# Kernel optimization log

Hardware: AMD Instinct MI355X
Metric: run time of the kernel (lower is better)

Reference implementation:

```python
import jax, jax.numpy as jnp
import numpy as np

NUM_K_HEADS = 16
NUM_V_HEADS = 32
DK = 128
DV = 128
KCONV = 4
EPS = 1e-6
KEY_DIM = NUM_K_HEADS * DK      # 2048
VALUE_DIM = NUM_V_HEADS * DV    # 4096
HIDDEN = 2048
T_TOKENS = 4096


def setup_inputs() -> dict:
    key = jax.random.key(0)
    ks = jax.random.split(key, 10)
    s = 0.02
    return {
        "hidden_states": jax.random.normal(ks[0], (T_TOKENS, HIDDEN), jnp.float32),
        "W_qkv": jax.random.normal(ks[1], (2 * KEY_DIM + VALUE_DIM, HIDDEN), jnp.float32) * s,
        "W_z": jax.random.normal(ks[2], (VALUE_DIM, HIDDEN), jnp.float32) * s,
        "W_b": jax.random.normal(ks[3], (NUM_V_HEADS, HIDDEN), jnp.float32) * s,
        "W_a": jax.random.normal(ks[4], (NUM_V_HEADS, HIDDEN), jnp.float32) * s,
        "conv_weight": jax.random.normal(ks[5], (2 * KEY_DIM + VALUE_DIM, KCONV), jnp.float32) * 0.2,
        "dt_bias": jnp.ones((NUM_V_HEADS,), jnp.float32),
        "A_log": jax.random.normal(ks[6], (NUM_V_HEADS,), jnp.float32) * 0.5,
        "norm_weight": jnp.ones((DV,), jnp.float32),
        "W_out": jax.random.normal(ks[7], (HIDDEN, VALUE_DIM), jnp.float32) * s,
    }


def _l2norm(x):
    return x * jax.lax.rsqrt(jnp.sum(x * x, axis=-1, keepdims=True) + 1e-6)


def _gdn_forward(hidden_states, W_qkv, W_z, W_b, W_a, conv_weight,
                 dt_bias, A_log, norm_weight, W_out):
    T = hidden_states.shape[0]
    # input projections
    mixed_qkv = hidden_states @ W_qkv.T                         # [T, 2K+V]
    z = (hidden_states @ W_z.T).reshape(T, NUM_V_HEADS, DV)     # gate
    b = hidden_states @ W_b.T                                   # [T, Hv]
    a = hidden_states @ W_a.T                                   # [T, Hv]

    # depthwise causal conv1d (kernel 4) + silu, no bias
    xp = jnp.pad(mixed_qkv, ((KCONV - 1, 0), (0, 0)))
    conv = sum(xp[i:i + T] * conv_weight[:, i] for i in range(KCONV))
    x = jax.nn.silu(conv)

    q = x[:, :KEY_DIM].reshape(T, NUM_K_HEADS, DK)
    k = x[:, KEY_DIM:2 * KEY_DIM].reshape(T, NUM_K_HEADS, DK)
    v = x[:, 2 * KEY_DIM:].reshape(T, NUM_V_HEADS, DV)

    rep = NUM_V_HEADS // NUM_K_HEADS  # grouped value attention: repeat q/k heads
    q = jnp.repeat(_l2norm(q), rep, axis=1)  # [T, Hv, DK]
    k = jnp.repeat(_l2norm(k), rep, axis=1)

    beta = jax.nn.sigmoid(b)                                   # [T, Hv]
    g = -jnp.exp(A_log) * jax.nn.softplus(a + dt_bias)         # [T, Hv] log-decay
    scale = DK ** -0.5

    def step(S, inp):
        qt, kt, vt, bt, gt = inp
        S = S * jnp.exp(gt)[:, None, None]                     # gated decay
        kv = jnp.einsum('hk,hkv->hv', kt, S)                   # memory readout
        delta = (vt - kv) * bt[:, None]                        # delta rule update
        S = S + jnp.einsum('hk,hv->hkv', kt, delta)
        ot = jnp.einsum('hk,hkv->hv', qt, S) * scale
        return S, ot

    S0 = jnp.zeros((NUM_V_HEADS, DK, DV), mixed_qkv.dtype)
    _, o = jax.lax.scan(step, S0, (q, k, v, beta, g))          # o: [T, Hv, DV]

    # gated RMSNorm (norm before gate)
    var = jnp.mean(o * o, axis=-1, keepdims=True)
    on = o * jax.lax.rsqrt(var + EPS) * norm_weight
    y = on * jax.nn.silu(z)

    return y.reshape(T, VALUE_DIM) @ W_out.T                   # [T, HIDDEN]


def reference(hidden_states, W_qkv, W_z, W_b, W_a, conv_weight,
              dt_bias, A_log, norm_weight, W_out):
    return _gdn_forward(hidden_states, W_qkv, W_z, W_b, W_a, conv_weight,
                        dt_bias, A_log, norm_weight, W_out)
```

## Files before the change

kernel.cpp:

```cpp
#include <hip/hip_runtime.h>
#include <cstdint>
#include <cstddef>

typedef __bf16 bf16_t;
typedef __bf16 bf16x8 __attribute__((ext_vector_type(8)));
typedef __bf16 bf16x4 __attribute__((ext_vector_type(4)));
typedef float floatx4 __attribute__((ext_vector_type(4)));

__device__ __forceinline__ void async16(const bf16_t* g, bf16_t* l) {
  __builtin_amdgcn_global_load_lds(
      (const __attribute__((address_space(1))) unsigned int*)g,
      (__attribute__((address_space(3))) unsigned int*)l, 16, 0, 0);
}

__device__ __forceinline__ void barrier_lds() {
  asm volatile("s_waitcnt lgkmcnt(0)\n\ts_barrier" ::: "memory");
}

__device__ __forceinline__ float siluf(float x) { return x / (1.f + __expf(-x)); }

#define MFMA16(a, b, c) __builtin_amdgcn_mfma_f32_16x16x32_bf16(a, b, c, 0, 0, 0)
#define WAITV(n) asm volatile("s_waitcnt vmcnt(" #n ")" ::: "memory")
#define SBAR() asm volatile("s_barrier" ::: "memory")

__global__ __launch_bounds__(256) void k_cvt(const float* __restrict__ in,
                                             bf16_t* __restrict__ out, int n4) {
  int i = blockIdx.x * 256 + threadIdx.x;
  if (i >= n4) return;
  const float4 f = ((const float4*)in)[i];
  bf16x4 r;
  r[0] = (bf16_t)f.x; r[1] = (bf16_t)f.y; r[2] = (bf16_t)f.z; r[3] = (bf16_t)f.w;
  ((bf16x4*)out)[i] = r;
}

__global__ __launch_bounds__(256) void k_build_wba(const float* __restrict__ wb,
                                                   const float* __restrict__ wa,
                                                   bf16_t* __restrict__ out) {
  int i = blockIdx.x * 256 + threadIdx.x;
  int e = i * 4;
  int row = e >> 11;
  int col = e & 2047;
  float4 f = make_float4(0.f, 0.f, 0.f, 0.f);
  if (row < 32)      f = *(const float4*)&wb[row * 2048 + col];
  else if (row < 64) f = *(const float4*)&wa[(row - 32) * 2048 + col];
  bf16x4 r;
  r[0] = (bf16_t)f.x; r[1] = (bf16_t)f.y; r[2] = (bf16_t)f.z; r[3] = (bf16_t)f.w;
  *(bf16x4*)&out[e] = r;
}

template<bool OUT_BF16>
__global__ __launch_bounds__(256) void gemm_bt(const bf16_t* __restrict__ A,
                                               const bf16_t* __restrict__ B,
                                               void* __restrict__ Cout,
                                               int M, int N, int K) {
  __shared__ __align__(16) bf16_t As[4096];
  __shared__ __align__(16) bf16_t Bs[4096];
  const int tid  = threadIdx.x;
  const int lane = tid & 63;
  const int wave = tid >> 6;
  const int quad = lane >> 4;
  const int l16  = lane & 15;
  const int wr   = (wave >> 1) * 64;
  const int wc   = (wave & 1) * 64;
  const int m0   = blockIdx.y * 128;
  const int n0   = blockIdx.x * 128;
  const int ra   = tid >> 2;
  const int ca   = (tid & 3) * 8;

  const bf16_t* gA = A + (size_t)(m0 + ra) * K + ca;
  const bf16_t* gB = B + (size_t)(n0 + ra) * K + ca;
  bf16_t* lA = &As[tid * 8];
  bf16_t* lB = &Bs[tid * 8];

  floatx4 acc[4][4] = {};

  for (int k0 = 0; k0 < K; k0 += 32) {
    __syncthreads();
    async16(gA + k0, lA);
    async16(gA + k0 + (size_t)64 * K, lA + 2048);
    async16(gB + k0, lB);
    async16(gB + k0 + (size_t)64 * K, lB + 2048);
    __syncthreads();
    bf16x8 af[4], bfr[4];
#pragma unroll
    for (int i = 0; i < 4; ++i) {
      af[i]  = *(const bf16x8*)&As[(wr + i * 16 + l16) * 32 + quad * 8];
      bfr[i] = *(const bf16x8*)&Bs[(wc + i * 16 + l16) * 32 + quad * 8];
    }
#pragma unroll
    for (int mi = 0; mi < 4; ++mi)
#pragma unroll
      for (int ni = 0; ni < 4; ++ni)
        acc[mi][ni] = MFMA16(af[mi], bfr[ni], acc[mi][ni]);
  }

#pragma unroll
  for (int mi = 0; mi < 4; ++mi) {
#pragma unroll
    for (int ni = 0; ni < 4; ++ni) {
      const int row = m0 + wr + mi * 16 + quad * 4;
      const int col = n0 + wc + ni * 16 + l16;
#pragma unroll
      for (int r = 0; r < 4; ++r) {
        if (OUT_BF16)
          ((bf16_t*)Cout)[(size_t)(row + r) * N + col] = (bf16_t)acc[mi][ni][r];
        else
          ((float*)Cout)[(size_t)(row + r) * N + col] = acc[mi][ni][r];
      }
    }
  }
}

__global__ __launch_bounds__(512, 1) void gemm8p(const bf16_t* __restrict__ A,
                                                 const bf16_t* __restrict__ B,
                                                 bf16_t* __restrict__ C0,
                                                 bf16_t* __restrict__ C1,
                                                 int M, int N, int K, int NSPLIT) {
  extern __shared__ __align__(16) bf16_t sm[];
  const int tid  = threadIdx.x;
  const int lane = tid & 63;
  const int wave = tid >> 6;
  const int quad = lane >> 4;
  const int l16  = lane & 15;
  const int wm   = wave >> 2;
  const int wn   = wave & 3;

  const int gx  = (int)gridDim.x;
  const int nwg = gx * (int)gridDim.y;
  const int id  = (int)blockIdx.y * gx + (int)blockIdx.x;
  const int cpx = nwg >> 3;
  const int sw  = (id & 7) * cpx + (id >> 3);
  const int m0  = (sw / gx) * 256;
  const int n0  = (sw % gx) * 256;

  const int rowg   = tid >> 3;
  const int colsrc = (tid & 7) ^ (rowg & 7);
  const bf16_t* gAs = A + (size_t)(m0 + rowg) * K + colsrc * 8;
  const bf16_t* gBs = B + (size_t)(n0 + rowg) * K + colsrc * 8;
  bf16_t* lds0 = sm + tid * 8;

#define STG_A8(u, kt, ht) {                                     \
    bf16_t* la = lds0 + (u) * 32768 + (ht) * 8192;              \
    const bf16_t* ga = gAs + (size_t)(ht) * 128 * K + (kt) * 64;\
    async16(ga, la); async16(ga + (size_t)64 * K, la + 4096); }
#define STG_B8(u, kt, ht) {                                     \
    bf16_t* lb = lds0 + (u) * 32768 + 16384 + (ht) * 8192;      \
    const bf16_t* gb = gBs + (size_t)(ht) * 128 * K + (kt) * 64;\
    async16(gb, lb); async16(gb + (size_t)64 * K, lb + 4096); }

  const int x7  = l16 & 7;
  const int cA0 = ((quad + 0) ^ x7) * 8;
  const int cA1 = ((quad + 4) ^ x7) * 8;
  const int eA0 = (wm * 128 + l16) * 64;
  const int eB0 = 16384 + (wn * 64 + l16) * 64;

  floatx4 acc[8][4] = {};
  const int KT = K >> 6;

  STG_A8(0, 0, 0); STG_A8(0, 0, 1);
  STG_B8(0, 0, 0); STG_B8(0, 0, 1);
  STG_B8(1, 1, 0); STG_B8(1, 1, 1);
  WAITV(4);
  SBAR();

  bf16x8 af[4][2], bn0[2][2], bn1[2][2];
  for (int X = 0; X < KT; ++X) {
    const int c = X & 1;
    const bf16_t* sb = sm + c * 32768;

#pragma unroll
    for (int i = 0; i < 4; ++i) {
      af[i][0] = *(const bf16x8*)&sb[eA0 + i * 1024 + cA0];
      af[i][1] = *(const bf16x8*)&sb[eA0 + i * 1024 + cA1];
    }
#pragma unroll
    for (int j = 0; j < 2; ++j) {
      bn0[j][0] = *(const bf16x8*)&sb[eB0 + j * 1024 + cA0];
      bn0[j][1] = *(const bf16x8*)&sb[eB0 + j * 1024 + cA1];
    }
    if (X + 1 < KT) STG_A8(c ^ 1, X + 1, 0);
    SBAR();
    __builtin_amdgcn_s_setprio(1);
#pragma unroll
    for (int i = 0; i < 4; ++i)
#pragma unroll
      for (int j = 0; j < 2; ++j) {
        acc[i][j] = MFMA16(af[i][0], bn0[j][0], acc[i][j]);
        acc[i][j] = MFMA16(af[i][1], bn0[j][1], acc[i][j]);
      }
    __builtin_amdgcn_s_setprio(0);
    SBAR();

#pragma unroll
    for (int j = 0; j < 2; ++j) {
      bn1[j][0] = *(const bf16x8*)&sb[eB0 + (2 + j) * 1024 + cA0];
      bn1[j][1] = *(const bf16x8*)&sb[eB0 + (2 + j) * 1024 + cA1];
    }
    if (X + 1 < KT) STG_A8(c ^ 1, X + 1, 1);
    SBAR();
    __builtin_amdgcn_s_setprio(1);
#pragma unroll
    for (int i = 0; i < 4; ++i)
#pragma unroll
      for (int j = 0; j < 2; ++j) {
        acc[i][2 + j] = MFMA16(af[i][0], bn1[j][0], acc[i][2 + j]);
        acc[i][2 + j] = MFMA16(af[i][1], bn1[j][1], acc[i][2 + j]);
      }
    __builtin_amdgcn_s_setprio(0);
    SBAR();

#pragma unroll
    for (int i = 0; i < 4; ++i) {
      af[i][0] = *(const bf16x8*)&sb[eA0 + (4 + i) * 1024 + cA0];
      af[i][1] = *(const bf16x8*)&sb[eA0 + (4 + i) * 1024 + cA1];
    }
    if (X + 2 < KT) STG_B8(c, X + 2, 0);
    SBAR();
    __builtin_amdgcn_s_setprio(1);
#pragma unroll
    for (int i = 0; i < 4; ++i)
#pragma unroll
      for (int j = 0; j < 2; ++j) {
        acc[4 + i][j] = MFMA16(af[i][0], bn0[j][0], acc[4 + i][j]);
        acc[4 + i][j] = MFMA16(af[i][1], bn0[j][1], acc[4 + i][j]);
      }
    __builtin_amdgcn_s_setprio(0);
    SBAR();

    if (X + 2 < KT) { STG_B8(c, X + 2, 1); WAITV(4); }
    else            { WAITV(0); }
    SBAR();
    __builtin_amdgcn_s_setprio(1);
#pragma unroll
    for (int i = 0; i < 4; ++i)
#pragma unroll
      for (int j = 0; j < 2; ++j) {
        acc[4 + i][2 + j] = MFMA16(af[i][0], bn1[j][0], acc[4 + i][2 + j]);
        acc[4 + i][2 + j] = MFMA16(af[i][1], bn1[j][1], acc[4 + i][2 + j]);
      }
    __builtin_amdgcn_s_setprio(0);
    SBAR();
  }
#undef STG_A8
#undef STG_B8

  const bool lo = (n0 < NSPLIT);
  bf16_t* Cb = lo ? C0 : C1;
  const int pitch = lo ? NSPLIT : (N - NSPLIT);
  const int ncol0 = lo ? n0 : (n0 - NSPLIT);
#pragma unroll
  for (int mi = 0; mi < 8; ++mi) {
#pragma unroll
    for (int ni = 0; ni < 4; ++ni) {
      const int row = m0 + wm * 128 + mi * 16 + quad * 4;
      const int col = ncol0 + wn * 64 + ni * 16 + l16;
#pragma unroll
      for (int r = 0; r < 4; ++r)
        Cb[(size_t)(row + r) * pitch + col] = (bf16_t)acc[mi][ni][r];
    }
  }
}

template<int MH, bool OUT_BF16>
__global__ __launch_bounds__(512, 1) void gemm_big(const bf16_t* __restrict__ A,
                                                   const bf16_t* __restrict__ B,
                                                   void* __restrict__ Cout,
                                                   int M, int N, int K) {
  extern __shared__ __align__(16) bf16_t sm[];
  constexpr int BM    = MH * 128;
  constexpr int MFRAG = MH * 4;
  constexpr int HF    = MFRAG / 2;
  constexpr int BUFE  = MH * 4096 + 8192;
  const int tid  = threadIdx.x;
  const int lane = tid & 63;
  const int wave = tid >> 6;
  const int quad = lane >> 4;
  const int l16  = lane & 15;
  const int wm   = wave >> 2;
  const int wn   = wave & 3;

  const int gx  = (int)gridDim.x;
  const int nwg = gx * (int)gridDim.y;
  const int id  = (int)blockIdx.y * gx + (int)blockIdx.x;
  const int cpx = nwg >> 3;
  const int sw  = (id & 7) * cpx + (id >> 3);
  const int m0  = (sw / gx) * BM;
  const int n0  = (sw % gx) * 256;

  const int lr    = lane >> 2;
  const int lslot = (lane & 3) ^ ((lane >> 3) & 3);
  const bf16_t* gA = A + (size_t)(m0 + wave * (MH * 16) + lr) * K + lslot * 8;
  const bf16_t* gB = B + (size_t)(n0 + wave * 32 + lr) * K + lslot * 8;
  const int ldsA0 = wave * (MH * 512) + lane * 8;
  const int ldsB0 = MH * 4096 + wave * 1024 + lane * 8;

#define STG_A(u, kt) {                                          \
    bf16_t* la = sm + (u) * BUFE + ldsA0;                       \
    const bf16_t* ga = gA + (size_t)(kt) * 32;                  \
    async16(ga, la);                                            \
    if constexpr (MH == 2) async16(ga + (size_t)16 * K, la + 512); }
#define STG_B(u, kt) {                                          \
    bf16_t* lb = sm + (u) * BUFE + ldsB0;                       \
    const bf16_t* gb = gB + (size_t)(kt) * 32;                  \
    async16(gb, lb);                                            \
    async16(gb + (size_t)16 * K, lb + 512); }

  int offA[MFRAG], offB[4];
#pragma unroll
  for (int i = 0; i < MFRAG; ++i) {
    int ra = wm * (MFRAG * 16) + i * 16 + l16;
    offA[i] = (ra * 32 + quad * 8) ^ (((ra >> 1) & 3) << 3);
  }
#pragma unroll
  for (int i = 0; i < 4; ++i) {
    int rb = wn * 64 + i * 16 + l16;
    offB[i] = MH * 4096 + ((rb * 32 + quad * 8) ^ (((rb >> 1) & 3) << 3));
  }

  floatx4 acc[MFRAG][4] = {};
  const int KT = K >> 5;

  STG_A(0, 0); STG_B(0, 0);
  STG_A(1, 1); STG_B(1, 1);
  STG_A(2, 2); STG_B(2, 2);
  if constexpr (MH == 2) WAITV(8); else WAITV(6);
  SBAR();

  for (int U = 0; U < KT; ++U) {
    const int bu = U & 3;
    const bf16_t* sb = sm + bu * BUFE;
    const int un = U + 3;
    const int tu = un & 3;
    bf16x8 af[HF], bfr[4];

#pragma unroll
    for (int i = 0; i < HF; ++i) af[i] = *(const bf16x8*)&sb[offA[i]];
#pragma unroll
    for (int i = 0; i < 4; ++i) bfr[i] = *(const bf16x8*)&sb[offB[i]];
    if (un < KT) STG_A(tu, un);
    SBAR();
    __builtin_amdgcn_s_setprio(1);
#pragma unroll
    for (int mi = 0; mi < HF; ++mi)
#pragma unroll
      for (int ni = 0; ni < 4; ++ni)
        acc[mi][ni] = MFMA16(af[mi], bfr[ni], acc[mi][ni]);
    __builtin_amdgcn_s_setprio(0);
    SBAR();

#pragma unroll
    for (int i = 0; i < HF; ++i) af[i] = *(const bf16x8*)&sb[offA[HF + i]];
    if (un < KT) STG_B(tu, un);
    if (un < KT)         { if constexpr (MH == 2) WAITV(8); else WAITV(6); }
    else if (U + 2 < KT) { if constexpr (MH == 2) WAITV(4); else WAITV(3); }
    else                 WAITV(0);
    SBAR();
    __builtin_amdgcn_s_setprio(1);
#pragma unroll
    for (int mi = 0; mi < HF; ++mi)
#pragma unroll
      for (int ni = 0; ni < 4; ++ni)
        acc[HF + mi][ni] = MFMA16(af[mi], bfr[ni], acc[HF + mi][ni]);
    __builtin_amdgcn_s_setprio(0);
    SBAR();
  }
#undef STG_A
#undef STG_B

#pragma unroll
  for (int mi = 0; mi < MFRAG; ++mi) {
#pragma unroll
    for (int ni = 0; ni < 4; ++ni) {
      const int row = m0 + wm * (MFRAG * 16) + mi * 16 + quad * 4;
      const int col = n0 + wn * 64 + ni * 16 + l16;
#pragma unroll
      for (int r = 0; r < 4; ++r) {
        if (OUT_BF16)
          ((bf16_t*)Cout)[(size_t)(row + r) * N + col] = (bf16_t)acc[mi][ni][r];
        else
          ((float*)Cout)[(size_t)(row + r) * N + col] = acc[mi][ni][r];
      }
    }
  }
}

__global__ __launch_bounds__(256) void k_betag(const float* __restrict__ cba,
                                               const float* __restrict__ A_log,
                                               const float* __restrict__ dtb,
                                               float* __restrict__ beta_t,
                                               float* __restrict__ g_t) {
  int i = blockIdx.x * 256 + threadIdx.x;
  int t = i >> 5, h = i & 31;
  float b = cba[t * 128 + h];
  float a = cba[t * 128 + 32 + h];
  beta_t[h * 4096 + t] = 1.f / (1.f + __expf(-b));
  float x = a + dtb[h];
  float sp = (x > 20.f) ? x : log1pf(__expf(x));
  g_t[h * 4096 + t] = -__expf(A_log[h]) * sp;
}

__global__ __launch_bounds__(64) void k_conv(const bf16_t* __restrict__ mixed,
                                             const float* __restrict__ cw,
                                             bf16_t* __restrict__ qo,
                                             bf16_t* __restrict__ ko,
                                             bf16_t* __restrict__ vo) {
  const int grp = blockIdx.x;
  const int t0 = blockIdx.y * 8;
  const int l = threadIdx.x;
  const int c0 = grp * 128 + l;
  const int c1 = c0 + 64;
  const float4 w0 = *(const float4*)&cw[c0 * 4];
  const float4 w1 = *(const float4*)&cw[c1 * 4];
  float h0[3], h1[3];
#pragma unroll
  for (int j = 0; j < 3; ++j) {
    int tt = t0 - 3 + j;
    h0[j] = (tt >= 0) ? (float)mixed[(size_t)tt * 8192 + c0] : 0.f;
    h1[j] = (tt >= 0) ? (float)mixed[(size_t)tt * 8192 + c1] : 0.f;
  }
#pragma unroll
  for (int i = 0; i < 8; ++i) {
    const int t = t0 + i;
    float x0 = (float)mixed[(size_t)t * 8192 + c0];
    float x1 = (float)mixed[(size_t)t * 8192 + c1];
    float a0 = w0.x * h0[0] + w0.y * h0[1] + w0.z * h0[2] + w0.w * x0;
    float a1 = w1.x * h1[0] + w1.y * h1[1] + w1.z * h1[2] + w1.w * x1;
    h0[0] = h0[1]; h0[1] = h0[2]; h0[2] = x0;
    h1[0] = h1[1]; h1[1] = h1[2]; h1[2] = x1;
    float v0 = siluf(a0), v1 = siluf(a1);
    if (grp < 32) {
      float s = v0 * v0 + v1 * v1;
#pragma unroll
      for (int m = 1; m < 64; m <<= 1) s += __shfl_xor(s, m);
      float r = rsqrtf(s + 1e-6f);
      if (grp < 16) {
        bf16_t* q = qo + ((size_t)t * 16 + grp) * 128;
        q[l]      = (bf16_t)(v0 * r * 0.08838834764831845f);
        q[l + 64] = (bf16_t)(v1 * r * 0.08838834764831845f);
      } else {
        bf16_t* k = ko + ((size_t)t * 16 + grp - 16) * 128;
        k[l]      = (bf16_t)(v0 * r);
        k[l + 64] = (bf16_t)(v1 * r);
      }
    } else {
      bf16_t* v = vo + ((size_t)t * 32 + grp - 32) * 128;
      v[l]      = (bf16_t)v0;
      v[l + 64] = (bf16_t)v1;
    }
  }
}

__global__ __launch_bounds__(256, 2) void k_prep(
    const bf16_t* __restrict__ qg, const bf16_t* __restrict__ kg,
    const bf16_t* __restrict__ vg,
    const float* __restrict__ bb_t, const float* __restrict__ gb_t,
    bf16_t* __restrict__ Vt, bf16_t* __restrict__ Wlo, bf16_t* __restrict__ Whi,
    bf16_t* __restrict__ Mout, bf16_t* __restrict__ kt, float* __restrict__ smalls) {
  const int c = blockIdx.x >> 5;
  const int h = blockIdx.x & 31;
  const int kh = h >> 1;
  const int t0 = c * 64;
  const int tid = threadIdx.x, lane = tid & 63, wave = tid >> 6;
  const int quad = lane >> 4, l16 = lane & 15;

  __shared__ __align__(16) bf16_t lsKQ[2][64][136];
  __shared__ float lsC[64][68];
  __shared__ float lsG[64], lsA[64], lsSc[64], lsBeta[64];

  {
    const int r = tid >> 2, s0 = (tid & 3) * 32;
    const bf16_t* kr = kg + ((size_t)(t0 + r) * 16 + kh) * 128 + s0;
    const bf16_t* qr = qg + ((size_t)(t0 + r) * 16 + kh) * 128 + s0;
#pragma unroll
    for (int j = 0; j < 4; ++j) {
      *(uint4*)&lsKQ[0][r][s0 + j * 8] = *(const uint4*)&kr[j * 8];
      *(uint4*)&lsKQ[1][r][s0 + j * 8] = *(const uint4*)&qr[j * 8];
    }
  }
  if (wave == 0) {
    float gv = gb_t[(size_t)h * 4096 + t0 + lane];
#pragma unroll
    for (int off = 1; off < 64; off <<= 1) {
      float n = __shfl_up(gv, off);
      if (lane >= off) gv += n;
    }
    float GL = __shfl(gv, 63);
    lsG[lane] = gv;
    lsA[lane] = __expf(gv);
    lsSc[lane] = __expf(GL - gv);
    lsBeta[lane] = bb_t[(size_t)h * 4096 + t0 + lane];
  }
  __syncthreads();

  const int mr = (wave >> 1) * 32, nr = (wave & 1) * 32;
  floatx4 ak[2][2] = {}, aq[2][2] = {};
  if (wave != 1) {
#pragma unroll
    for (int ks = 0; ks < 4; ++ks) {
      bf16x8 yf[2], xk[2], xq[2];
#pragma unroll
      for (int i = 0; i < 2; ++i) {
        yf[i] = *(const bf16x8*)&lsKQ[0][nr + i * 16 + l16][ks * 32 + quad * 8];
        xk[i] = *(const bf16x8*)&lsKQ[0][mr + i * 16 + l16][ks * 32 + quad * 8];
        xq[i] = *(const bf16x8*)&lsKQ[1][mr + i * 16 + l16][ks * 32 + quad * 8];
      }
#pragma unroll
      for (int i = 0; i < 2; ++i)
#pragma unroll
        for (int j = 0; j < 2; ++j) {
          ak[i][j] = MFMA16(xk[i], yf[j], ak[i][j]);
          aq[i][j] = MFMA16(xq[i], yf[j], aq[i][j]);
        }
    }
  }
  bf16_t* Mb = Mout + (size_t)(h * 64 + c) * 4096;
#pragma unroll
  for (int i = 0; i < 2; ++i)
#pragma unroll
    for (int j = 0; j < 2; ++j)
#pragma unroll
      for (int r = 0; r < 4; ++r) {
        int t = mr + i * 16 + quad * 4 + r;
        int s = nr + j * 16 + l16;
        float e = __expf(lsG[t] - lsG[s]);
        float cv = (s < t) ? lsBeta[t] * e * ak[i][j][r] : 0.f;
        float mv = (s <= t) ? e * aq[i][j][r] : 0.f;
        if (wave != 1) lsC[t][s] = cv;
        Mb[t * 64 + s] = (bf16_t)mv;
      }
  __syncthreads();

  const int col = tid & 127;
  const bool isW = tid >= 128;
  float vals[64];
#pragma unroll
  for (int t = 0; t < 64; ++t) {
    float b;
    if (!isW) b = (float)vg[((size_t)(t0 + t) * 32 + h) * 128 + col];
    else      b = lsA[t] * (float)lsKQ[0][t][col];
    vals[t] = lsBeta[t] * b;
  }
#pragma unroll
  for (int t = 1; t < 64; ++t) {
    float acc = vals[t];
#pragma unroll
    for (int s4 = 0; s4 <= (t - 1) >> 2; ++s4) {
      float4 cv = *(const float4*)&lsC[t][s4 * 4];
      acc -= cv.x * vals[s4 * 4 + 0];
      acc -= cv.y * vals[s4 * 4 + 1];
      acc -= cv.z * vals[s4 * 4 + 2];
      acc -= cv.w * vals[s4 * 4 + 3];
    }
    vals[t] = acc;
  }

  if (!isW) {
    bf16_t* vd = Vt + (size_t)(h * 64 + c) * 8192 + (size_t)col * 64;
#pragma unroll
    for (int j = 0; j < 16; ++j) {
      bf16x4 p;
      p[0] = (bf16_t)vals[j * 4 + 0];
      p[1] = (bf16_t)vals[j * 4 + 1];
      p[2] = (bf16_t)vals[j * 4 + 2];
      p[3] = (bf16_t)vals[j * 4 + 3];
      *(bf16x4*)&vd[j * 4] = p;
    }
  } else {
#pragma unroll
    for (int t = 0; t < 64; ++t) vals[t] = -vals[t];
  }

  if ((h & 1) == 0) {
    const int dk = tid >> 1, sh = (tid & 1) * 32;
    bf16_t* kd = kt + (size_t)(c * 16 + kh) * 8192 + (size_t)dk * 64 + sh;
#pragma unroll
    for (int j4 = 0; j4 < 4; ++j4) {
      bf16x8 v;
#pragma unroll
      for (int e = 0; e < 8; ++e) v[e] = lsKQ[0][sh + j4 * 8 + e][dk];
      *(bf16x8*)&kd[j4 * 8] = v;
    }
  }
  if (tid < 64) {
    float* sm = smalls + (size_t)(h * 64 + c) * 128;
    sm[tid] = lsA[tid];
    sm[64 + tid] = lsSc[tid];
  }
  __syncthreads();

  bf16_t* lsT = &lsKQ[0][0][0];
  if (isW) {
#pragma unroll
    for (int t = 0; t < 64; ++t) lsT[t * 272 + tid] = (bf16_t)vals[t];
  }
  __syncthreads();

  {
    const int r = tid >> 2, part = tid & 3;
    const bf16_t* src = &lsT[r * 272 + 128 + part * 32];
    bf16_t* Wb = (h < 16 ? Wlo : Whi) + (size_t)((h & 15) * 64 + c) * 8192 + r * 128 + part * 32;
#pragma unroll
    for (int j = 0; j < 4; ++j)
      *(uint4*)&Wb[j * 8] = *(const uint4*)&src[j * 8];
  }
}

__global__ __launch_bounds__(256, 1) void k_chain(
    const bf16_t* __restrict__ qg, const bf16_t* __restrict__ VtT,
    const bf16_t* __restrict__ Wlo, const bf16_t* __restrict__ Whi,
    const bf16_t* __restrict__ Mg, const bf16_t* __restrict__ ktg,
    const float* __restrict__ smalls, bf16_t* __restrict__ o) {
  const int h = blockIdx.x & 31;
  const int dv0 = (blockIdx.x >> 5) * 16;
  const int kh = h >> 1;
  const int tid = threadIdx.x, lane = tid & 63, wave = tid >> 6;
  const int quad = lane >> 4, l16 = lane & 15;
  const int trow = wave * 16 + quad * 4;

  __shared__ __align__(16) bf16_t lsXT[16][72];
  __shared__ __align__(16) bf16_t lsXbT[16][72];
  __shared__ __align__(16) bf16_t lsS[16][136];

  const bf16_t* Wbase = (h < 16 ? Wlo : Whi) + (size_t)(h & 15) * 64 * 8192;
  const bf16_t* Vbase = VtT + (size_t)h * 64 * 8192;
  const bf16_t* Mbase = Mg + (size_t)h * 64 * 4096;
  const float*  Sbase = smalls + (size_t)h * 64 * 128;

  const bf16_t* pW = Wbase + (size_t)(wave * 16 + l16) * 128 + quad * 8;
  const bf16_t* pQ = qg + ((size_t)(wave * 16 + l16) * 16 + kh) * 128 + quad * 8;
  const bf16_t* pK = ktg + (size_t)kh * 8192 + (size_t)(wave * 16 + l16) * 64 + quad * 8;
  const bf16_t* pM = Mbase + (size_t)(wave * 16 + l16) * 64 + quad * 8;
  const bf16_t* pV = Vbase + (size_t)(dv0 + l16) * 64 + trow;
  const float*  pS = Sbase;

  floatx4 sacc[2] = {};
  for (int i = tid; i < 16 * 136; i += 256) (&lsS[0][0])[i] = (bf16_t)0.f;

  bf16x8 nW[4], nQ[4], nK[4], nM[2];
  bf16x4 nV;
  float4 nA, nSc;
  float nAL;
  {
#pragma unroll
    for (int ks = 0; ks < 4; ++ks) {
      nW[ks] = *(const bf16x8*)&pW[ks * 32];
      nQ[ks] = *(const bf16x8*)&pQ[ks * 32];
    }
    nK[0] = *(const bf16x8*)&pK[0];
    nK[1] = *(const bf16x8*)&pK[32];
    nK[2] = *(const bf16x8*)&pK[4096];
    nK[3] = *(const bf16x8*)&pK[4096 + 32];
    nM[0] = *(const bf16x8*)&pM[0];
    nM[1] = *(const bf16x8*)&pM[32];
    nV = *(const bf16x4*)&pV[0];
    nA  = *(const float4*)&pS[trow];
    nSc = *(const float4*)&pS[64 + trow];
    nAL = pS[63];
    pW += 8192; pQ += 131072; pK += 131072; pM += 4096; pV += 8192; pS += 128;
  }
  __syncthreads();

  for (int cc = 0; cc < 64; ++cc) {
    const int t0 = cc * 64;
    bf16x8 cW[4], cQ[4], cK[4], cM[2];
    float cV[4];
    float4 cA = nA, cSc = nSc;
    float cAL = nAL;
#pragma unroll
    for (int ks = 0; ks < 4; ++ks) { cW[ks] = nW[ks]; cQ[ks] = nQ[ks]; cK[ks] = nK[ks]; }
    cM[0] = nM[0]; cM[1] = nM[1];
#pragma unroll
    for (int r = 0; r < 4; ++r) cV[r] = (float)nV[r];

    if (cc + 1 < 64) {
#pragma unroll
      for (int ks = 0; ks < 4; ++ks) {
        nW[ks] = *(const bf16x8*)&pW[ks * 32];
        nQ[ks] = *(const bf16x8*)&pQ[ks * 32];
      }
      nK[0] = *(const bf16x8*)&pK[0];
      nK[1] = *(const bf16x8*)&pK[32];
      nK[2] = *(const bf16x8*)&pK[4096];
      nK[3] = *(const bf16x8*)&pK[4096 + 32];
      nM[0] = *(const bf16x8*)&pM[0];
      nM[1] = *(const bf16x8*)&pM[32];
      nV = *(const bf16x4*)&pV[0];
      nA  = *(const float4*)&pS[trow];
      nSc = *(const float4*)&pS[64 + trow];
      nAL = pS[63];
      pW += 8192; pQ += 131072; pK += 131072; pM += 4096; pV += 8192; pS += 128;
    }

    bf16x8 bS[4];
#pragma unroll
    for (int ks = 0; ks < 4; ++ks)
      bS[ks] = *(const bf16x8*)&lsS[l16][ks * 32 + quad * 8];
    floatx4 xacc;
#pragma unroll
    for (int r = 0; r < 4; ++r) xacc[r] = cV[r];
#pragma unroll
    for (int ks = 0; ks < 4; ++ks)
      xacc = MFMA16(cW[ks], bS[ks], xacc);
    {
      bf16x4 px, pb;
#pragma unroll
      for (int r = 0; r < 4; ++r) {
        px[r] = (bf16_t)xacc[r];
        pb[r] = (bf16_t)(xacc[r] * ((const float*)&cSc)[r]);
      }
      *(bf16x4*)&lsXT[l16][trow] = px;
      *(bf16x4*)&lsXbT[l16][trow] = pb;
    }
    floatx4 qacc = {};
#pragma unroll
    for (int ks = 0; ks < 4; ++ks)
      qacc = MFMA16(cQ[ks], bS[ks], qacc);
#pragma unroll
    for (int r = 0; r < 4; ++r) qacc[r] *= ((const float*)&cA)[r];
#pragma unroll
    for (int mh = 0; mh < 2; ++mh)
#pragma unroll
      for (int r = 0; r < 4; ++r) sacc[mh][r] *= cAL;
    barrier_lds();

#pragma unroll
    for (int ks = 0; ks < 2; ++ks) {
      bf16x8 bX = *(const bf16x8*)&lsXT[l16][ks * 32 + quad * 8];
      qacc = MFMA16(cM[ks], bX, qacc);
    }
#pragma unroll
    for (int r = 0; r < 4; ++r)
      o[((size_t)(t0 + trow + r) * 32 + h) * 128 + dv0 + l16] = (bf16_t)qacc[r];

#pragma unroll
    for (int ks = 0; ks < 2; ++ks) {
      bf16x8 bXb = *(const bf16x8*)&lsXbT[l16][ks * 32 + quad * 8];
#pragma unroll
      for (int mh = 0; mh < 2; ++mh)
        sacc[mh] = MFMA16(cK[mh * 2 + ks], bXb, sacc[mh]);
    }
#pragma unroll
    for (int mh = 0; mh < 2; ++mh) {
      bf16x4 ps;
#pragma unroll
      for (int r = 0; r < 4; ++r) ps[r] = (bf16_t)sacc[mh][r];
      *(bf16x4*)&lsS[l16][(wave + 4 * mh) * 16 + quad * 4] = ps;
    }
    barrier_lds();
  }
}

__global__ __launch_bounds__(256) void k_gate(const bf16_t* __restrict__ o,
                                              const bf16_t* __restrict__ z,
                                              const float* __restrict__ nw,
                                              bf16_t* __restrict__ y) {
  const int row = blockIdx.x * 4 + (threadIdx.x >> 6);
  const int l = threadIdx.x & 63;
  const bf16_t* orow = o + (size_t)row * 128;
  float o0 = (float)orow[l], o1 = (float)orow[l + 64];
  float s = o0 * o0 + o1 * o1;
#pragma unroll
  for (int m = 1; m < 64; m <<= 1) s += __shfl_xor(s, m);
  float r = rsqrtf(s * (1.f / 128.f) + 1e-6f);
  const bf16_t* zrow = z + (size_t)row * 128;
  float z0 = (float)zrow[l], z1 = (float)zrow[l + 64];
  bf16_t* yrow = y + (size_t)row * 128;
  yrow[l]      = (bf16_t)(o0 * r * nw[l] * siluf(z0));
  yrow[l + 64] = (bf16_t)(o1 * r * nw[l + 64] * siluf(z1));
}

extern "C" void kernel_launch(void* const* d_in, const int* in_sizes, int n_in,
                              void* d_out, int out_size, void* d_ws, size_t ws_size,
                              hipStream_t stream) {
  const float* hidden = (const float*)d_in[0];
  const float* W_qkv  = (const float*)d_in[1];
  const float* W_z    = (const float*)d_in[2];
  const float* W_b    = (const float*)d_in[3];
  const float* W_a    = (const float*)d_in[4];
  const float* conv_w = (const float*)d_in[5];
  const float* dt_b   = (const float*)d_in[6];
  const float* A_log  = (const float*)d_in[7];
  const float* norm_w = (const float*)d_in[8];
  const float* W_out  = (const float*)d_in[9];
  float* out = (float*)d_out;

  static int gemm_attr_done = 0;
  if (!gemm_attr_done) {
    hipFuncSetAttribute(reinterpret_cast<const void*>(&gemm8p),
                        hipFuncAttributeMaxDynamicSharedMemorySize, 131072);
    hipFuncSetAttribute(reinterpret_cast<const void*>(&gemm_big<1, false>),
                        hipFuncAttributeMaxDynamicSharedMemorySize, 98304);
    gemm_attr_done = 1;
  }

  char* w = (char*)d_ws;
  const size_t MB = 1024 * 1024;
  bf16_t* hs    = (bf16_t*)(w + 0 * MB);
  bf16_t* Wlo   = hs;
  bf16_t* wqkv  = (bf16_t*)(w + 16 * MB);
  bf16_t* Vtb   = wqkv;
  bf16_t* ybuf  = wqkv;
  bf16_t* wz    = (bf16_t*)(w + 48 * MB);
  bf16_t* Whi   = wz;
  bf16_t* wout  = (bf16_t*)(w + 64 * MB);
  bf16_t* wba   = (bf16_t*)(w + 80 * MB);
  bf16_t* mixed = (bf16_t*)(w + 81 * MB);
  bf16_t* obuf  = mixed;
  bf16_t* Mbuf  = (bf16_t*)(w + 113 * MB);
  bf16_t* ktb   = (bf16_t*)(w + 129 * MB);
  bf16_t* zbuf  = (bf16_t*)(w + 145 * MB);
  float*  cba   = (float*)(w + 177 * MB);
  float*  smalls= cba;
  bf16_t* qb    = (bf16_t*)(w + 179 * MB);
  bf16_t* kb    = (bf16_t*)(w + 195 * MB);
  bf16_t* vb    = (bf16_t*)(w + 211 * MB);
  float*  betab = (float*)(w + 243 * MB);
  float*  gbuf  = (float*)(w + 243 * MB + 512 * 1024);

  k_cvt<<<8192, 256, 0, stream>>>(hidden, hs, 2097152);
  k_cvt<<<16384, 256, 0, stream>>>(W_qkv, wqkv, 4194304);
  k_cvt<<<8192, 256, 0, stream>>>(W_z, wz, 2097152);
  k_cvt<<<8192, 256, 0, stream>>>(W_out, wout, 2097152);
  k_build_wba<<<256, 256, 0, stream>>>(W_b, W_a, wba);

  gemm8p<<<dim3(48, 16), 512, 131072, stream>>>(hs, wqkv, mixed, zbuf,
                                                4096, 12288, 2048, 8192);
  gemm_bt<false><<<dim3(1, 32), 256, 0, stream>>>(hs, wba, cba, 4096, 128, 2048);
  k_betag<<<512, 256, 0, stream>>>(cba, A_log, dt_b, betab, gbuf);

  k_conv<<<dim3(64, 512), 64, 0, stream>>>(mixed, conv_w, qb, kb, vb);

  k_prep<<<2048, 256, 0, stream>>>(qb, kb, vb, betab, gbuf,
                                   Vtb, Wlo, Whi, Mbuf, ktb, smalls);
  k_chain<<<256, 256, 0, stream>>>(qb, Vtb, Wlo, Whi, Mbuf, ktb, smalls, obuf);

  k_gate<<<32768, 256, 0, stream>>>(obuf, zbuf, norm_w, ybuf);
  gemm_big<1, false><<<dim3(8, 32), 512, 98304, stream>>>(ybuf, wout, out, 4096, 2048, 4096);
}
```

Before: 816.8 us.

## Retune GEMM tile swizzle and move vmcnt wait after final MFMA phase

Adds a hardcoded tile-to-workgroup mapping for the 48x16 grid case so each group of eight interleaved workgroups covers a compact block of M and N tiles, aiming for better L2 reuse. Replaces per-stage address recomputation with incrementing global pointers and precomputed row strides. Moves the vmcnt wait for the next stage's loads from before the last MFMA block to after it, so those loads overlap more compute, and adds a partial lgkmcnt wait before the first barrier. The special-case mapping holds only for one grid shape, and the changed wait placement carries a risk of LDS read/write hazards.

New measurement: 810.8 us. About the same (-0.7%).

```diff
diff --git a/kernel.cpp b/kernel.cpp
--- a/kernel.cpp
+++ b/kernel.cpp
@@ -126,27 +126,37 @@
   const int wn   = wave & 3;
 
   const int gx  = (int)gridDim.x;
-  const int nwg = gx * (int)gridDim.y;
+  const int gy  = (int)gridDim.y;
   const int id  = (int)blockIdx.y * gx + (int)blockIdx.x;
-  const int cpx = nwg >> 3;
-  const int sw  = (id & 7) * cpx + (id >> 3);
-  const int m0  = (sw / gx) * 256;
-  const int n0  = (sw % gx) * 256;
+  int m0, n0;
+  if (gx == 48 && gy == 16) {
+    const int x8 = id & 7, j = id >> 3;
+    m0 = ((x8 & 1) * 8 + (j & 7)) * 256;
+    n0 = ((x8 >> 1) * 12 + (j >> 3)) * 256;
+  } else {
+    const int nwg = gx * gy, cpx = nwg >> 3;
+    const int sw = (id & 7) * cpx + (id >> 3);
+    m0 = (sw / gx) * 256;
+    n0 = (sw % gx) * 256;
+  }
 
   const int rowg   = tid >> 3;
   const int colsrc = (tid & 7) ^ (rowg & 7);
   const bf16_t* gAs = A + (size_t)(m0 + rowg) * K + colsrc * 8;
   const bf16_t* gBs = B + (size_t)(n0 + rowg) * K + colsrc * 8;
   bf16_t* lds0 = sm + tid * 8;
+  const size_t rowK = (size_t)K;
+  const size_t H64  = rowK * 64;
+  const size_t H128 = rowK * 128;
 
 #define STG_A8(u, kt, ht) {                                     \
     bf16_t* la = lds0 + (u) * 32768 + (ht) * 8192;              \
-    const bf16_t* ga = gAs + (size_t)(ht) * 128 * K + (kt) * 64;\
-    async16(ga, la); async16(ga + (size_t)64 * K, la + 4096); }
+    const bf16_t* ga = gAs + (size_t)(ht) * H128 + (kt) * 64;   \
+    async16(ga, la); async16(ga + H64, la + 4096); }
 #define STG_B8(u, kt, ht) {                                     \
     bf16_t* lb = lds0 + (u) * 32768 + 16384 + (ht) * 8192;      \
-    const bf16_t* gb = gBs + (size_t)(ht) * 128 * K + (kt) * 64;\
-    async16(gb, lb); async16(gb + (size_t)64 * K, lb + 4096); }
+    const bf16_t* gb = gBs + (size_t)(ht) * H128 + (kt) * 64;   \
+    async16(gb, lb); async16(gb + H64, lb + 4096); }
 
   const int x7  = l16 & 7;
   const int cA0 = ((quad + 0) ^ x7) * 8;
@@ -163,10 +173,17 @@
   WAITV(4);
   SBAR();
 
+  const bf16_t* pAs = gAs + 64;
+  const bf16_t* pBs = gBs + 128;
+
   bf16x8 af[4][2], bn0[2][2], bn1[2][2];
   for (int X = 0; X < KT; ++X) {
     const int c = X & 1;
     const bf16_t* sb = sm + c * 32768;
+    bf16_t* dA = lds0 + (c ^ 1) * 32768;
+    bf16_t* dB = lds0 + c * 32768 + 16384;
+    const bool stgA = (X + 1 < KT);
+    const bool stgB = (X + 2 < KT);
 
 #pragma unroll
     for (int i = 0; i < 4; ++i) {
@@ -178,7 +195,8 @@
       bn0[j][0] = *(const bf16x8*)&sb[eB0 + j * 1024 + cA0];
       bn0[j][1] = *(const bf16x8*)&sb[eB0 + j * 1024 + cA1];
     }
-    if (X + 1 < KT) STG_A8(c ^ 1, X + 1, 0);
+    if (stgA) { async16(pAs, dA); async16(pAs + H64, dA + 4096); }
+    asm volatile("s_waitcnt lgkmcnt(8)" ::: "memory");
     SBAR();
     __builtin_amdgcn_s_setprio(1);
 #pragma unroll
@@ -196,7 +214,10 @@
       bn1[j][0] = *(const bf16x8*)&sb[eB0 + (2 + j) * 1024 + cA0];
       bn1[j][1] = *(const bf16x8*)&sb[eB0 + (2 + j) * 1024 + cA1];
     }
-    if (X + 1 < KT) STG_A8(c ^ 1, X + 1, 1);
+    if (stgA) {
+      const bf16_t* g = pAs + H128;
+      async16(g, dA + 8192); async16(g + H64, dA + 8192 + 4096);
+    }
     SBAR();
     __builtin_amdgcn_s_setprio(1);
 #pragma unroll
@@ -214,7 +235,7 @@
       af[i][0] = *(const bf16x8*)&sb[eA0 + (4 + i) * 1024 + cA0];
       af[i][1] = *(const bf16x8*)&sb[eA0 + (4 + i) * 1024 + cA1];
     }
-    if (X + 2 < KT) STG_B8(c, X + 2, 0);
+    if (stgB) { async16(pBs, dB); async16(pBs + H64, dB + 4096); }
     SBAR();
     __builtin_amdgcn_s_setprio(1);
 #pragma unroll
@@ -227,8 +248,10 @@
     __builtin_amdgcn_s_setprio(0);
     SBAR();
 
-    if (X + 2 < KT) { STG_B8(c, X + 2, 1); WAITV(4); }
-    else            { WAITV(0); }
+    if (stgB) {
+      const bf16_t* g = pBs + H128;
+      async16(g, dB + 8192); async16(g + H64, dB + 8192 + 4096);
+    }
     SBAR();
     __builtin_amdgcn_s_setprio(1);
 #pragma unroll
@@ -239,7 +262,11 @@
         acc[4 + i][2 + j] = MFMA16(af[i][1], bn1[j][1], acc[4 + i][2 + j]);
       }
     __builtin_amdgcn_s_setprio(0);
-    SBAR();
+    if (stgB) WAITV(4);
+    else      WAITV(0);
+    SBAR();
+
+    pAs += 64; pBs += 64;
   }
 #undef STG_A8
 #undef STG_B8
```
